# Optimization experiments

Measured on AMD Instinct MI355X. Metric: run time of the kernel, lower is better.

## Reference

```python
import jax, jax.numpy as jnp
import numpy as np


def fwht(x):
    """Fast Walsh-Hadamard transform along axis 1 of a (B, n, D) array.
    Unnormalized, matches the torch butterfly: (a+b, a-b) per stage."""
    B, n, D = x.shape
    h = 1
    y = x
    while h < n:  # log2(n) static stages
        # group axis-1 into blocks of 2*h: (B, n//(2h), 2, h, D)
        y = y.reshape(B, n // (2 * h), 2, h, D)
        a = y[:, :, 0]
        b = y[:, :, 1]
        y = jnp.stack((a + b, a - b), axis=2).reshape(B, n, D)
        h *= 2
    return y


def setup_inputs() -> dict:
    key = jax.random.key(0)
    x = jax.random.normal(key, (64, 1024, 512), dtype=jnp.float32)
    return {"x": x}


def reference(x):
    return fwht(x)
```

## Files before the change

### kernel.cpp

```cpp
#include <hip/hip_runtime.h>


constexpr int NB = 64;
constexpr int NR = 1024;
constexpr int ND = 512;
constexpr int DC = 32;
constexpr int TPB = 512;
constexpr int GRID = 256;
constexpr int TPT = (NB * (ND / DC)) / GRID;

#define BAR() asm volatile("s_waitcnt lgkmcnt(0)\n\ts_barrier" ::: "memory")

__global__ __launch_bounds__(TPB, 2)
void fwht_kernel(const float* __restrict__ x, float* __restrict__ y) {
    __shared__ float lds[NR * DC];

    const int tid = threadIdx.x;
    const int pid = blockIdx.x;
    const int b   = pid & 63;
    const int dg0 = pid >> 6;

    const int g  = tid >> 3;
    const int w  = tid & 7;
    const int j2 = tid >> 5;
    const int c  = tid & 31;

    const size_t rowA = ((size_t)b * NR + (size_t)g * 16) * ND + (size_t)(w * 4);

    float4 v[16];
    {
        const float* src = x + rowA + dg0 * DC;
#pragma unroll
        for (int j = 0; j < 16; ++j)
            v[j] = *reinterpret_cast<const float4*>(src + (size_t)j * ND);
    }

#pragma unroll
    for (int t = 0; t < TPT; ++t) {
        const int dbase = (dg0 + 4 * t) * DC;

        float4 vn[16];
        if (t < TPT - 1) {
            const float* srcn = x + rowA + (dbase + 4 * DC);
#pragma unroll
            for (int j = 0; j < 16; ++j)
                vn[j] = *reinterpret_cast<const float4*>(srcn + (size_t)j * ND);
        }

#pragma unroll
        for (int hb = 1; hb < 16; hb <<= 1) {
#pragma unroll
            for (int j = 0; j < 16; ++j) {
                if ((j & hb) == 0) {
                    const int k = j | hb;
                    float4 a = v[j], bb = v[k];
                    v[j] = make_float4(a.x + bb.x, a.y + bb.y, a.z + bb.z, a.w + bb.w);
                    v[k] = make_float4(a.x - bb.x, a.y - bb.y, a.z - bb.z, a.w - bb.w);
                }
            }
        }

        {
            float4* lp = reinterpret_cast<float4*>(lds) + (size_t)g * 128 + w;
#pragma unroll
            for (int j = 0; j < 16; ++j)
                lp[j * 8] = v[j];
        }
        BAR();

        float u[64];
#pragma unroll
        for (int i = 0; i < 64; ++i)
            u[i] = lds[i * 512 + j2 * 32 + c];

#pragma unroll
        for (int hb = 1; hb < 64; hb <<= 1) {
#pragma unroll
            for (int i = 0; i < 64; ++i) {
                if ((i & hb) == 0) {
                    const int k = i | hb;
                    float a = u[i], bb = u[k];
                    u[i] = a + bb;
                    u[k] = a - bb;
                }
            }
        }
        BAR();

#pragma unroll
        for (int i = 0; i < 64; ++i)
            lds[i * 512 + j2 * 32 + c] = u[i];
        BAR();

        {
            float* dst = y + rowA + dbase;
            const float4* lp = reinterpret_cast<const float4*>(lds) + (size_t)g * 128 + w;
#pragma unroll
            for (int j = 0; j < 16; ++j)
                *reinterpret_cast<float4*>(dst + (size_t)j * ND) = lp[j * 8];
        }
        BAR();

        if (t < TPT - 1) {
#pragma unroll
            for (int j = 0; j < 16; ++j) v[j] = vn[j];
        }
    }
}

extern "C" void kernel_launch(void* const* d_in, const int* in_sizes, int n_in,
                              void* d_out, int out_size, void* d_ws, size_t ws_size,
                              hipStream_t stream) {
    const float* x = (const float*)d_in[0];
    float* y = (float*)d_out;
    fwht_kernel<<<dim3(GRID), dim3(TPB), 0, stream>>>(x, y);
}
```

Baseline: 243.6 us.

## Split FWHT into two streaming global-memory passes without shared memory

Replaces the single LDS-based kernel with two kernels. The first does a 64-point transform over rows within each 64-row segment. The second does the remaining 16-point stage across segments in place on the output. This removes shared-memory transposes and barriers and raises the block count for better latency hiding, but it doubles global memory traffic.

```diff
diff --git a/kernel.cpp b/kernel.cpp
--- a/kernel.cpp
+++ b/kernel.cpp
@@ -4,108 +4,66 @@
 constexpr int NB = 64;
 constexpr int NR = 1024;
 constexpr int ND = 512;
-constexpr int DC = 32;
-constexpr int TPB = 512;
-constexpr int GRID = 256;
-constexpr int TPT = (NB * (ND / DC)) / GRID;
 
-#define BAR() asm volatile("s_waitcnt lgkmcnt(0)\n\ts_barrier" ::: "memory")
+__global__ __launch_bounds__(512)
+void fwht_k1(const float* __restrict__ x, float* __restrict__ y) {
+    const int c   = threadIdx.x;
+    const int sid = blockIdx.x;
+    const size_t base = (size_t)sid * (64 * ND) + (size_t)c;
 
-__global__ __launch_bounds__(TPB, 2)
-void fwht_kernel(const float* __restrict__ x, float* __restrict__ y) {
-    __shared__ float lds[NR * DC];
+    float u[64];
+#pragma unroll
+    for (int i = 0; i < 64; ++i)
+        u[i] = x[base + (size_t)i * ND];
 
-    const int tid = threadIdx.x;
-    const int pid = blockIdx.x;
-    const int b   = pid & 63;
-    const int dg0 = pid >> 6;
-
-    const int g  = tid >> 3;
-    const int w  = tid & 7;
-    const int j2 = tid >> 5;
-    const int c  = tid & 31;
-
-    const size_t rowA = ((size_t)b * NR + (size_t)g * 16) * ND + (size_t)(w * 4);
-
-    float4 v[16];
-    {
-        const float* src = x + rowA + dg0 * DC;
 #pragma unroll
-        for (int j = 0; j < 16; ++j)
-            v[j] = *reinterpret_cast<const float4*>(src + (size_t)j * ND);
+    for (int hb = 1; hb < 64; hb <<= 1) {
+#pragma unroll
+        for (int i = 0; i < 64; ++i) {
+            if ((i & hb) == 0) {
+                const int k = i | hb;
+                float a = u[i], bb = u[k];
+                u[i] = a + bb;
+                u[k] = a - bb;
+            }
+        }
     }
 
 #pragma unroll
-    for (int t = 0; t < TPT; ++t) {
-        const int dbase = (dg0 + 4 * t) * DC;
+    for (int i = 0; i < 64; ++i)
+        y[base + (size_t)i * ND] = u[i];
+}
 
-        float4 vn[16];
-        if (t < TPT - 1) {
-            const float* srcn = x + rowA + (dbase + 4 * DC);
+__global__ __launch_bounds__(128)
+void fwht_k2(float* __restrict__ y) {
+    const int q   = threadIdx.x;
+    const int pid = blockIdx.x;
+    const int b   = pid >> 6;
+    const int r   = pid & 63;
+    const size_t base = ((size_t)b * NR + (size_t)r) * ND + (size_t)(q * 4);
+    constexpr size_t RSTEP = (size_t)64 * ND;
+
+    float4 v[16];
 #pragma unroll
-            for (int j = 0; j < 16; ++j)
-                vn[j] = *reinterpret_cast<const float4*>(srcn + (size_t)j * ND);
-        }
+    for (int g = 0; g < 16; ++g)
+        v[g] = *reinterpret_cast<const float4*>(&y[base + (size_t)g * RSTEP]);
 
 #pragma unroll
-        for (int hb = 1; hb < 16; hb <<= 1) {
+    for (int hb = 1; hb < 16; hb <<= 1) {
 #pragma unroll
-            for (int j = 0; j < 16; ++j) {
-                if ((j & hb) == 0) {
-                    const int k = j | hb;
-                    float4 a = v[j], bb = v[k];
-                    v[j] = make_float4(a.x + bb.x, a.y + bb.y, a.z + bb.z, a.w + bb.w);
-                    v[k] = make_float4(a.x - bb.x, a.y - bb.y, a.z - bb.z, a.w - bb.w);
-                }
+        for (int g = 0; g < 16; ++g) {
+            if ((g & hb) == 0) {
+                const int k = g | hb;
+                float4 a = v[g], bb = v[k];
+                v[g] = make_float4(a.x + bb.x, a.y + bb.y, a.z + bb.z, a.w + bb.w);
+                v[k] = make_float4(a.x - bb.x, a.y - bb.y, a.z - bb.z, a.w - bb.w);
             }
         }
-
-        {
-            float4* lp = reinterpret_cast<float4*>(lds) + (size_t)g * 128 + w;
-#pragma unroll
-            for (int j = 0; j < 16; ++j)
-                lp[j * 8] = v[j];
-        }
-        BAR();
-
-        float u[64];
-#pragma unroll
-        for (int i = 0; i < 64; ++i)
-            u[i] = lds[i * 512 + j2 * 32 + c];
+    }
 
 #pragma unroll
-        for (int hb = 1; hb < 64; hb <<= 1) {
-#pragma unroll
-            for (int i = 0; i < 64; ++i) {
-                if ((i & hb) == 0) {
-                    const int k = i | hb;
-                    float a = u[i], bb = u[k];
-                    u[i] = a + bb;
-                    u[k] = a - bb;
-                }
-            }
-        }
-        BAR();
-
-#pragma unroll
-        for (int i = 0; i < 64; ++i)
-            lds[i * 512 + j2 * 32 + c] = u[i];
-        BAR();
-
-        {
-            float* dst = y + rowA + dbase;
-            const float4* lp = reinterpret_cast<const float4*>(lds) + (size_t)g * 128 + w;
-#pragma unroll
-            for (int j = 0; j < 16; ++j)
-                *reinterpret_cast<float4*>(dst + (size_t)j * ND) = lp[j * 8];
-        }
-        BAR();
-
-        if (t < TPT - 1) {
-#pragma unroll
-            for (int j = 0; j < 16; ++j) v[j] = vn[j];
-        }
-    }
+    for (int g = 0; g < 16; ++g)
+        *reinterpret_cast<float4*>(&y[base + (size_t)g * RSTEP]) = v[g];
 }
 
 extern "C" void kernel_launch(void* const* d_in, const int* in_sizes, int n_in,
@@ -113,5 +71,6 @@
                               hipStream_t stream) {
     const float* x = (const float*)d_in[0];
     float* y = (float*)d_out;
-    fwht_kernel<<<dim3(GRID), dim3(TPB), 0, stream>>>(x, y);
+    fwht_k1<<<dim3(NB * (NR / 64)), dim3(512), 0, stream>>>(x, y);
+    fwht_k2<<<dim3(NB * 64), dim3(128), 0, stream>>>(y);
 }
```

Result: slower. 265.7 us (+9.1%).
